# Performance work log

Measured on AMD Instinct MI355X. Metric: run time of the kernel, lower is better.

## Reference

```python
import jax, jax.numpy as jnp
import numpy as np

NUM_SAMPLES = 100


def setup_inputs() -> dict:
    key = jax.random.key(0)
    # [B, 2C, H, W]: first C channels are logits, last C are log-std
    inp = jax.random.normal(key, (8, 38, 256, 256), dtype=jnp.float32)
    return {"input": inp}


def reference(input):
    logits, log_std = jnp.split(input, 2, axis=-3)  # each [B, C, H, W]
    std = jnp.exp(log_std)
    keys = jax.random.split(jax.random.key(1), NUM_SAMPLES)

    def body(acc, k):
        eps = jax.random.normal(k, std.shape, dtype=std.dtype)
        acc = acc + jax.nn.softmax(logits + eps * std, axis=-3)
        return acc, None

    softmax_sum, _ = jax.lax.scan(body, jnp.zeros_like(logits), keys)
    return softmax_sum / NUM_SAMPLES
```

## Files before the change

### kernel.cpp

```cpp
#include <hip/hip_runtime.h>
#include <hip/hip_fp16.h>
#include <stdint.h>


#define NCH    19
#define HW     65536
#define NSAMP  100

__device__ __forceinline__ uint32_t rotl(uint32_t x, uint32_t r) {
  return __builtin_amdgcn_alignbit(x, x, 32u - r);
}

__device__ __forceinline__ void tf2x32_full(uint32_t k0, uint32_t k1,
                                            uint32_t x0, uint32_t x1,
                                            uint32_t& o0, uint32_t& o1) {
  const uint32_t k2 = k0 ^ k1 ^ 0x1BD11BDAu;
#define TFR(r) { x0 += x1; x1 = rotl(x1, r) ^ x0; }
  x0 += k0; x1 += k1;
  TFR(13u) TFR(15u) TFR(26u) TFR(6u)
  x0 += k1; x1 += k2 + 1u;
  TFR(17u) TFR(29u) TFR(16u) TFR(24u)
  x0 += k2; x1 += k0 + 2u;
  TFR(13u) TFR(15u) TFR(26u) TFR(6u)
  x0 += k0; x1 += k1 + 3u;
  TFR(17u) TFR(29u) TFR(16u) TFR(24u)
  x0 += k1; x1 += k2 + 4u;
  TFR(13u) TFR(15u) TFR(26u) TFR(6u)
  x0 += k2; x1 += k0 + 5u;
#undef TFR
  o0 = x0; o1 = x1;
}

__device__ __forceinline__ uint32_t tf_fold(uint32_t k0, uint32_t k1, uint32_t k2,
                                            uint32_t x1in) {
  uint32_t x0, x1;
  x1 = x1in + k1;
  x0 = k0 + x1;
  x1 = rotl(x1, 13u) ^ x0;
  x0 += x1; x1 = rotl(x1, 15u) ^ x0;
  x0 += x1; x1 = rotl(x1, 26u) ^ x0;
  x0 += x1; x1 = rotl(x1,  6u) ^ x0;
  x1 += k2 + 1u;
  x0 = x0 + k1 + x1; x1 = rotl(x1, 17u) ^ x0;
  x0 += x1; x1 = rotl(x1, 29u) ^ x0;
  x0 += x1; x1 = rotl(x1, 16u) ^ x0;
  x0 += x1; x1 = rotl(x1, 24u) ^ x0;
  x1 += k0 + 2u;
  x0 = x0 + k2 + x1; x1 = rotl(x1, 13u) ^ x0;
  x0 += x1; x1 = rotl(x1, 15u) ^ x0;
  x0 += x1; x1 = rotl(x1, 26u) ^ x0;
  x0 += x1; x1 = rotl(x1,  6u) ^ x0;
  x1 += k1 + 3u;
  x0 = x0 + k0 + x1; x1 = rotl(x1, 17u) ^ x0;
  x0 += x1; x1 = rotl(x1, 29u) ^ x0;
  x0 += x1; x1 = rotl(x1, 16u) ^ x0;
  x0 += x1; x1 = rotl(x1, 24u) ^ x0;
  x1 += k2 + 4u;
  x0 = x0 + k1 + x1; x1 = rotl(x1, 13u) ^ x0;
  x0 += x1; x1 = rotl(x1, 15u) ^ x0;
  x0 += x1; x1 = rotl(x1, 26u) ^ x0;
  x0 += x1; x1 = rotl(x1,  6u) ^ x0;
  return (x0 + k2) ^ (x1 + k0 + 5u);
}

__device__ __forceinline__ float bits_to_eps(uint32_t bits) {
  const float lo = -0.99999994f;
  float x = __uint_as_float((bits >> 9) | 0x3F800000u);
  float u = fmaf(x, 2.0f, -3.0f);
  u = fmaxf(u, lo);
  float t = __builtin_amdgcn_logf(fmaf(-u, u, 1.0f));
  float p;
  if (t > -7.2135401f) {
    float tw = t + 3.6067376f;
    p = 2.1176667e-09f;
    p = fmaf(p, tw, -3.7319753e-08f);
    p = fmaf(p, tw, -5.5262077e-07f);
    p = fmaf(p, tw, 9.9370361e-07f);
    p = fmaf(p, tw, 7.1355918e-05f);
    p = fmaf(p, tw, 5.9046852e-04f);
    p = fmaf(p, tw, -2.8386612e-03f);
    p = fmaf(p, tw, -2.4177230e-01f);
    p = fmaf(p, tw, 2.1233141e+00f);
  } else {
    float w = -0.69314718f * t;
    w = __fsqrt_rn(w) - 3.0f;
    p = -2.8314594e-04f;
    p = fmaf(p, w, 1.4276565e-04f);
    p = fmaf(p, w, 1.9082604e-03f);
    p = fmaf(p, w, -5.1950124e-03f);
    p = fmaf(p, w, 8.1168916e-03f);
    p = fmaf(p, w, -1.0779791e-02f);
    p = fmaf(p, w, 1.3348577e-02f);
    p = fmaf(p, w, 1.4165810e+00f);
    p = fmaf(p, w, 4.0064324e+00f);
  }
  return p * u;
}

__global__ void HS_keys_kernel(uint2* __restrict__ ks) {
  const int t = threadIdx.x;
  if (t < NSAMP) {
    uint32_t a, b;
    tf2x32_full(0u, 1u, 0u, (uint32_t)t, a, b);
    ks[t] = make_uint2(a, b);
  }
}

__global__ __launch_bounds__(256, 8)
void HeteroscedasticSoftmax_kernel(const float* __restrict__ in,
                                   float* __restrict__ out,
                                   const uint2* __restrict__ keys) {
  __shared__ __half2 sls[NCH][256];

  const int t   = threadIdx.x;
  const int gid = blockIdx.x * 256 + t;
  const int b_  = gid >> 16;
  const int hw  = gid & 65535;

  const float L2E = 1.4426950408889634f;
  const float* pin = in + (size_t)b_ * (2 * NCH * HW) + hw;
  float acc[NCH];
#pragma unroll
  for (int c = 0; c < NCH; ++c) {
    float lg = pin[c * HW] * L2E;
    float sd = __expf(pin[(NCH + c) * HW]) * L2E;
    sls[c][t] = __floats2half2_rn(lg, sd);
    acc[c] = 0.0f;
  }
  __syncthreads();

  const uint32_t jbase = (uint32_t)(b_ * NCH) * (uint32_t)HW + (uint32_t)hw;

#pragma unroll 1
  for (int s = 0; s < NSAMP; ++s) {
    const uint2 kk = keys[s];
    const uint32_t k0 = __builtin_amdgcn_readfirstlane(kk.x);
    const uint32_t k1 = __builtin_amdgcn_readfirstlane(kk.y);
    const uint32_t k2 = k0 ^ k1 ^ 0x1BD11BDAu;

    float z[NCH];
#pragma unroll
    for (int c = 0; c < NCH; ++c) {
      const uint32_t bits = tf_fold(k0, k1, k2, jbase + (uint32_t)c * HW);
      const float eps = bits_to_eps(bits);
      const __half2 h = sls[c][t];
      z[c] = fmaf(eps, __high2float(h), __low2float(h));
    }

    float m0 = fmaxf(z[0], z[1]),  m1 = fmaxf(z[2], z[3]);
    float m2 = fmaxf(z[4], z[5]),  m3 = fmaxf(z[6], z[7]);
    float m4 = fmaxf(z[8], z[9]),  m5 = fmaxf(z[10], z[11]);
    float m6 = fmaxf(z[12], z[13]), m7 = fmaxf(z[14], z[15]);
    float m8 = fmaxf(z[16], z[17]);
    m0 = fmaxf(m0, m1); m2 = fmaxf(m2, m3); m4 = fmaxf(m4, m5);
    m6 = fmaxf(m6, m7); m8 = fmaxf(m8, z[18]);
    m0 = fmaxf(m0, m2); m4 = fmaxf(m4, m6);
    m0 = fmaxf(m0, m4);
    const float m = fmaxf(m0, m8);

#pragma unroll
    for (int c = 0; c < NCH; ++c) z[c] = __builtin_amdgcn_exp2f(z[c] - m);

    float s0 = z[0] + z[1],  s1 = z[2] + z[3];
    float s2 = z[4] + z[5],  s3 = z[6] + z[7];
    float s4 = z[8] + z[9],  s5 = z[10] + z[11];
    float s6 = z[12] + z[13], s7 = z[14] + z[15];
    float s8 = z[16] + z[17];
    s0 += s1; s2 += s3; s4 += s5; s6 += s7; s8 += z[18];
    s0 += s2; s4 += s6;
    s0 += s4;
    const float r = __builtin_amdgcn_rcpf(s0 + s8);

#pragma unroll
    for (int c = 0; c < NCH; ++c) acc[c] = fmaf(z[c], r, acc[c]);
  }

  float* pout = out + (size_t)b_ * (NCH * HW) + hw;
#pragma unroll
  for (int c = 0; c < NCH; ++c) pout[c * HW] = acc[c] * 0.01f;
}

extern "C" void kernel_launch(void* const* d_in, const int* in_sizes, int n_in,
                              void* d_out, int out_size, void* d_ws, size_t ws_size,
                              hipStream_t stream) {
  const float* in = (const float*)d_in[0];
  float* out = (float*)d_out;
  uint2* keys = (uint2*)d_ws;
  HS_keys_kernel<<<1, 128, 0, stream>>>(keys);
  HeteroscedasticSoftmax_kernel<<<2048, 256, 0, stream>>>(in, out, keys);
}
```

Before: 2.246 ms.

## Split each pixel's channel softmax across two lanes with shuffle reductions

Each pixel is now handled by a pair of adjacent threads, each owning 10 of the 19 channels. A dummy 20th channel is padded with a very negative logit and zero std. Max and sum are combined across the pair with xor-shuffles, and the grid doubles to 4096 blocks. The aim is to double thread-level parallelism and cut per-thread register pressure, improving latency hiding in this compute-bound RNG/exp loop. The cost is one extra wasted Threefry/erfinv evaluation per pixel per sample, plus two shuffles per sample.

```diff
diff --git a/kernel.cpp b/kernel.cpp
--- a/kernel.cpp
+++ b/kernel.cpp
@@ -3,7 +3,6 @@
 #include <stdint.h>
 
 
-#define NCH    19
 #define HW     65536
 #define NSAMP  100
 
@@ -110,26 +109,35 @@
 void HeteroscedasticSoftmax_kernel(const float* __restrict__ in,
                                    float* __restrict__ out,
                                    const uint2* __restrict__ keys) {
-  __shared__ __half2 sls[NCH][256];
+  __shared__ __half2 sls[256][11];
 
-  const int t   = threadIdx.x;
-  const int gid = blockIdx.x * 256 + t;
-  const int b_  = gid >> 16;
-  const int hw  = gid & 65535;
+  const int t      = threadIdx.x;
+  const int parity = t & 1;
+  const int gp     = blockIdx.x * 128 + (t >> 1);
+  const int b_     = gp >> 16;
+  const int hw     = gp & 65535;
+  const int cbase  = parity * 10;
 
   const float L2E = 1.4426950408889634f;
-  const float* pin = in + (size_t)b_ * (2 * NCH * HW) + hw;
-  float acc[NCH];
+  const float* pin = in + (size_t)b_ * (2 * 19 * HW) + hw;
+  float acc[10];
 #pragma unroll
-  for (int c = 0; c < NCH; ++c) {
-    float lg = pin[c * HW] * L2E;
-    float sd = __expf(pin[(NCH + c) * HW]) * L2E;
-    sls[c][t] = __floats2half2_rn(lg, sd);
-    acc[c] = 0.0f;
+  for (int i = 0; i < 10; ++i) {
+    const int c = cbase + i;
+    float lg, sd;
+    if (c < 19) {
+      lg = pin[c * HW] * L2E;
+      sd = __expf(pin[(19 + c) * HW]) * L2E;
+    } else {
+      lg = -30000.0f;
+      sd = 0.0f;
+    }
+    sls[t][i] = __floats2half2_rn(lg, sd);
+    acc[i] = 0.0f;
   }
   __syncthreads();
 
-  const uint32_t jbase = (uint32_t)(b_ * NCH) * (uint32_t)HW + (uint32_t)hw;
+  const uint32_t jb2 = ((uint32_t)(b_ * 19 + cbase) << 16) + (uint32_t)hw;
 
 #pragma unroll 1
   for (int s = 0; s < NSAMP; ++s) {
@@ -138,46 +146,45 @@
     const uint32_t k1 = __builtin_amdgcn_readfirstlane(kk.y);
     const uint32_t k2 = k0 ^ k1 ^ 0x1BD11BDAu;
 
-    float z[NCH];
+    float z[10];
 #pragma unroll
-    for (int c = 0; c < NCH; ++c) {
-      const uint32_t bits = tf_fold(k0, k1, k2, jbase + (uint32_t)c * HW);
+    for (int i = 0; i < 10; ++i) {
+      const uint32_t bits = tf_fold(k0, k1, k2, jb2 + ((uint32_t)i << 16));
       const float eps = bits_to_eps(bits);
-      const __half2 h = sls[c][t];
-      z[c] = fmaf(eps, __high2float(h), __low2float(h));
+      const __half2 h = sls[t][i];
+      z[i] = fmaf(eps, __high2float(h), __low2float(h));
     }
 
-    float m0 = fmaxf(z[0], z[1]),  m1 = fmaxf(z[2], z[3]);
-    float m2 = fmaxf(z[4], z[5]),  m3 = fmaxf(z[6], z[7]);
-    float m4 = fmaxf(z[8], z[9]),  m5 = fmaxf(z[10], z[11]);
-    float m6 = fmaxf(z[12], z[13]), m7 = fmaxf(z[14], z[15]);
-    float m8 = fmaxf(z[16], z[17]);
-    m0 = fmaxf(m0, m1); m2 = fmaxf(m2, m3); m4 = fmaxf(m4, m5);
-    m6 = fmaxf(m6, m7); m8 = fmaxf(m8, z[18]);
-    m0 = fmaxf(m0, m2); m4 = fmaxf(m4, m6);
-    m0 = fmaxf(m0, m4);
-    const float m = fmaxf(m0, m8);
+    float m0 = fmaxf(z[0], z[1]), m1 = fmaxf(z[2], z[3]);
+    float m2 = fmaxf(z[4], z[5]), m3 = fmaxf(z[6], z[7]);
+    float m4 = fmaxf(z[8], z[9]);
+    m0 = fmaxf(m0, m1); m2 = fmaxf(m2, m3);
+    m0 = fmaxf(m0, m2);
+    float ml = fmaxf(m0, m4);
+    const float m = fmaxf(ml, __shfl_xor(ml, 1));
 
 #pragma unroll
-    for (int c = 0; c < NCH; ++c) z[c] = __builtin_amdgcn_exp2f(z[c] - m);
+    for (int i = 0; i < 10; ++i) z[i] = __builtin_amdgcn_exp2f(z[i] - m);
 
-    float s0 = z[0] + z[1],  s1 = z[2] + z[3];
-    float s2 = z[4] + z[5],  s3 = z[6] + z[7];
-    float s4 = z[8] + z[9],  s5 = z[10] + z[11];
-    float s6 = z[12] + z[13], s7 = z[14] + z[15];
-    float s8 = z[16] + z[17];
-    s0 += s1; s2 += s3; s4 += s5; s6 += s7; s8 += z[18];
-    s0 += s2; s4 += s6;
-    s0 += s4;
-    const float r = __builtin_amdgcn_rcpf(s0 + s8);
+    float s0 = z[0] + z[1], s1 = z[2] + z[3];
+    float s2 = z[4] + z[5], s3 = z[6] + z[7];
+    float s4 = z[8] + z[9];
+    s0 += s1; s2 += s3;
+    s0 += s2;
+    float sl = s0 + s4;
+    const float ssum = sl + __shfl_xor(sl, 1);
+    const float r = __builtin_amdgcn_rcpf(ssum);
 
 #pragma unroll
-    for (int c = 0; c < NCH; ++c) acc[c] = fmaf(z[c], r, acc[c]);
+    for (int i = 0; i < 10; ++i) acc[i] = fmaf(z[i], r, acc[i]);
   }
 
-  float* pout = out + (size_t)b_ * (NCH * HW) + hw;
+  float* pout = out + (size_t)b_ * (19 * HW) + hw;
 #pragma unroll
-  for (int c = 0; c < NCH; ++c) pout[c * HW] = acc[c] * 0.01f;
+  for (int i = 0; i < 10; ++i) {
+    const int c = cbase + i;
+    if (c < 19) pout[c * HW] = acc[i] * 0.01f;
+  }
 }
 
 extern "C" void kernel_launch(void* const* d_in, const int* in_sizes, int n_in,
@@ -187,5 +194,5 @@
   float* out = (float*)d_out;
   uint2* keys = (uint2*)d_ws;
   HS_keys_kernel<<<1, 128, 0, stream>>>(keys);
-  HeteroscedasticSoftmax_kernel<<<2048, 256, 0, stream>>>(in, out, keys);
+  HeteroscedasticSoftmax_kernel<<<4096, 256, 0, stream>>>(in, out, keys);
 }
```

After: 2.170 ms. 3.4% less time.
